# Performance work log

Measured on AMD Instinct MI355X. Metric: run time of the kernel, lower is better.

The kernel has to match this reference:

```python
import jax, jax.numpy as jnp
import numpy as np

ENT_FACTOR = 0.5  # entanglement_factor


def setup_inputs() -> dict:
    key = jax.random.key(0)
    k1, k2, k3, k4 = jax.random.split(key, 4)
    B, L, H, E = 2, 2048, 16, 128
    S = L
    return {
        "queries": jax.random.normal(k1, (B, L, H, E), dtype=jnp.float32),
        "keys": jax.random.normal(k2, (B, S, H, E), dtype=jnp.float32),
        "values": jax.random.normal(k3, (B, S, H, E), dtype=jnp.float32),
        "q_params": jax.random.uniform(k4, (4,), dtype=jnp.float32),
    }


def reference(queries, keys, values, q_params):
    B, L, H, E = queries.shape
    S = keys.shape[1]
    scale = 1.0 / jnp.sqrt(jnp.asarray(E, dtype=queries.dtype))
    # VQE circuit (RY layer, CNOT chain, <Z0>) reduces analytically to cos(theta0):
    # Z on the control qubit commutes with CNOT, so only RY(params[0]) matters.
    quantum_score = jnp.cos(q_params[0])
    # entanglement scores: values play the query role  -> [B,H,L,S]
    ent = jnp.einsum('blhd,bshd->bhls', values, keys)
    # NOTE: in QuantumAttentionOld classical QK scores are NOT added to `scores`.
    scores = quantum_score + ENT_FACTOR * ent
    causal = jnp.triu(jnp.ones((L, S), dtype=bool), k=1)  # True above diagonal
    scores = jnp.where(causal[None, None, :, :], -jnp.inf, scores)
    A = jax.nn.softmax(scale * scores, axis=-1)  # dropout is identity at eval
    V = jnp.einsum('bhls,bshd->blhd', A, values)
    return V
```

## Files before the change

### kernel.cpp

```cpp
#include <hip/hip_runtime.h>
#include <hip/hip_bf16.h>
#include <stdint.h>

#define LQ   2048
#define NH   16
#define DD   128
#define NB   2
#define QBLK 128
#define KBLK 64
#define NQT  (LQ/QBLK)
#define ROWSTR (NH*DD)

typedef float f32x4 __attribute__((ext_vector_type(4)));
typedef short s16x4 __attribute__((ext_vector_type(4)));
typedef short s16x8 __attribute__((ext_vector_type(8)));

__device__ __forceinline__ short f2bf(float f) {
  union { __hip_bfloat16 h; short s; } u;
  u.h = __float2bfloat16(f);
  return u.s;
}

__device__ __forceinline__ s16x4 cvt4(f32x4 x) {
  s16x4 r; r[0] = f2bf(x[0]); r[1] = f2bf(x[1]); r[2] = f2bf(x[2]); r[3] = f2bf(x[3]);
  return r;
}

__device__ __forceinline__ uint32_t lds_u32(const void* p) {
  return (uint32_t)(uint64_t)p;
}

__device__ __forceinline__ s16x4 tr16(uint32_t addr) {
  s16x4 d;
  asm volatile("ds_read_b64_tr_b16 %0, %1" : "=v"(d) : "v"(addr) : "memory");
  return d;
}

struct Stage { f32x4 k[4]; f32x4 v[4]; };

__device__ __forceinline__ Stage load_tile(const float* __restrict__ Kg,
                                           const float* __restrict__ Vg,
                                           int s0, int tid) {
  Stage st;
  const int rk = tid >> 5;
  const int c4 = tid & 31;
#pragma unroll
  for (int j = 0; j < 4; ++j)
    st.k[j] = *(const f32x4*)(Kg + (size_t)(s0 + rk + 16 * j) * ROWSTR + 4 * c4);
#pragma unroll
  for (int p = 0; p < 4; ++p) {
    const int g = tid + 512 * p;
    const int rv = (g & 3) | ((g >> 7) << 2);
    const int cv = (g >> 2) & 31;
    st.v[p] = *(const f32x4*)(Vg + (size_t)(s0 + rv) * ROWSTR + 4 * cv);
  }
  return st;
}

__device__ __forceinline__ void write_tile(short* Kb, short* Vb,
                                           const Stage& st, int tid) {
  const int rk = tid >> 5;
  const int c4 = tid & 31;
#pragma unroll
  for (int j = 0; j < 4; ++j)
    *(s16x4*)&Kb[(rk + 16 * j) * 132 + 4 * c4] = cvt4(st.k[j]);
#pragma unroll
  for (int p = 0; p < 4; ++p) {
    const int g = tid + 512 * p;
    const int rv = (g & 3) | ((g >> 7) << 2);
    const int cv = (g >> 2) & 31;
    const int sub = (rv >> 4) * 8 + (cv >> 2);
    *(s16x4*)&Vb[sub * 256 + (rv & 15) * 16 + 4 * (cv & 3)] = cvt4(st.v[p]);
  }
}

__global__ __launch_bounds__(512, 2) void qattn_fwd(
    const float* __restrict__ keys, const float* __restrict__ values,
    float* __restrict__ out)
{
  __shared__ short K_lds[2][KBLK * 132];
  __shared__ short V_lds[2][32 * 256];

  const int tid  = threadIdx.x;
  const int wid  = tid >> 6;
  const int lane = tid & 63;
  const int l15  = lane & 15;
  const int lhi  = lane >> 4;

  const int wg   = blockIdx.x;
  const int bh   = wg & 31;
  const int pair = wg >> 5;
  const int b    = bh >> 4;
  const int h    = bh & 15;

  const float* Kg = keys   + ((size_t)b * LQ * ROWSTR) + (size_t)h * DD;
  const float* Vg = values + ((size_t)b * LQ * ROWSTR) + (size_t)h * DD;
  float*       Og = out    + ((size_t)b * LQ * ROWSTR) + (size_t)h * DD;

  const float CS = 0.5f * 0.08838834764831845f * 1.4426950408889634f;

  for (int sp = 0; sp < 2; ++sp) {
    const int qt = sp ? (NQT - 1 - pair) : pair;
    const int q0 = qt * QBLK;
    const int nt = 2 * qt + 2;

    const int qg = q0 + wid * 16 + l15;
    const float* Qrow = Vg + (size_t)qg * ROWSTR;
    s16x8 qf[4];
#pragma unroll
    for (int c = 0; c < 4; ++c) {
      f32x4 lo = *(const f32x4*)(Qrow + 32 * c + 4 * lhi);
      f32x4 hi = *(const f32x4*)(Qrow + 32 * c + 16 + 4 * lhi);
      lo *= CS; hi *= CS;
      qf[c] = __builtin_shufflevector(cvt4(lo), cvt4(hi), 0, 1, 2, 3, 4, 5, 6, 7);
    }

    f32x4 o[8];
#pragma unroll
    for (int i = 0; i < 8; ++i) o[i] = f32x4{0.f, 0.f, 0.f, 0.f};
    float m  = -1e30f;
    float ll = 0.0f;
    const int q_wave_hi = q0 + wid * 16 + 15;

    {
      Stage st = load_tile(Kg, Vg, 0, tid);
      __syncthreads();
      write_tile(K_lds[0], V_lds[0], st, tid);
    }
    __syncthreads();

    for (int t = 0; t < nt; ++t) {
      const int cur = t & 1;
      const int s0  = t * KBLK;

      Stage st;
      const bool more = (t + 1) < nt;
      if (more) st = load_tile(Kg, Vg, (t + 1) * KBLK, tid);

      if (s0 <= q_wave_hi) {
        const short* Kb = K_lds[cur];
        short*       Vb = V_lds[cur];

        f32x4 sT[4];
#pragma unroll
        for (int sb = 0; sb < 4; ++sb) sT[sb] = f32x4{0.f, 0.f, 0.f, 0.f};
        __builtin_amdgcn_s_setprio(1);
#pragma unroll
        for (int c = 0; c < 4; ++c) {
#pragma unroll
          for (int sb = 0; sb < 4; ++sb) {
            s16x4 a = *(const s16x4*)&Kb[(sb * 16 + l15) * 132 + 32 * c + 4 * lhi];
            s16x4 bb = *(const s16x4*)&Kb[(sb * 16 + l15) * 132 + 32 * c + 16 + 4 * lhi];
            s16x8 kf = __builtin_shufflevector(a, bb, 0, 1, 2, 3, 4, 5, 6, 7);
            sT[sb] = __builtin_amdgcn_mfma_f32_16x16x32_bf16(kf, qf[c], sT[sb], 0, 0, 0);
          }
        }
        __builtin_amdgcn_s_setprio(0);

        float z[16];
#pragma unroll
        for (int sb = 0; sb < 4; ++sb)
#pragma unroll
          for (int r = 0; r < 4; ++r) z[sb * 4 + r] = sT[sb][r];
        if (s0 + KBLK - 1 > qg) {
#pragma unroll
          for (int sb = 0; sb < 4; ++sb)
#pragma unroll
            for (int r = 0; r < 4; ++r)
              if (s0 + sb * 16 + 4 * lhi + r > qg) z[sb * 4 + r] = -1e30f;
        }
        float tm = z[0];
#pragma unroll
        for (int i = 1; i < 16; ++i) tm = fmaxf(tm, z[i]);
        tm = fmaxf(tm, __shfl_xor(tm, 16));
        tm = fmaxf(tm, __shfl_xor(tm, 32));

        if (!__all(tm - m <= 8.0f)) {
          const float mn = fmaxf(m, tm);
          const float alpha = exp2f(m - mn);
          m = mn;
          float ar[4];
#pragma unroll
          for (int r = 0; r < 4; ++r) ar[r] = __shfl(alpha, 4 * lhi + r);
#pragma unroll
          for (int df = 0; df < 8; ++df)
#pragma unroll
            for (int r = 0; r < 4; ++r) o[df][r] *= ar[r];
          ll *= alpha;
        }
        float rs = 0.f;
        s16x8 pf0, pf1;
#pragma unroll
        for (int i = 0; i < 8; ++i) {
          float p = exp2f(z[i] - m);
          rs += p;
          pf0[i] = f2bf(p);
        }
#pragma unroll
        for (int i = 0; i < 8; ++i) {
          float p = exp2f(z[8 + i] - m);
          rs += p;
          pf1[i] = f2bf(p);
        }
        rs += __shfl_xor(rs, 16);
        rs += __shfl_xor(rs, 32);
        ll += rs;

        const uint32_t vbase = lds_u32(&Vb[0]) + 8u * (uint32_t)lane;
#pragma unroll
        for (int ks = 0; ks < 2; ++ks) {
          s16x4 vlo[8], vhi[8];
#pragma unroll
          for (int df = 0; df < 8; ++df) {
            vlo[df] = tr16(vbase + 512u * (uint32_t)(16 * ks + df));
            vhi[df] = tr16(vbase + 512u * (uint32_t)(16 * ks + 8 + df));
          }
          asm volatile("s_waitcnt lgkmcnt(0)" ::: "memory");
          __builtin_amdgcn_sched_barrier(0);
          const s16x8 pf = ks ? pf1 : pf0;
          __builtin_amdgcn_s_setprio(1);
#pragma unroll
          for (int df = 0; df < 8; ++df) {
            s16x8 vf = __builtin_shufflevector(vlo[df], vhi[df], 0, 1, 2, 3, 4, 5, 6, 7);
            o[df] = __builtin_amdgcn_mfma_f32_16x16x32_bf16(pf, vf, o[df], 0, 0, 0);
          }
          __builtin_amdgcn_s_setprio(0);
        }
      }

      if (more) write_tile(K_lds[cur ^ 1], V_lds[cur ^ 1], st, tid);
      __syncthreads();
    }

    const float linv = 1.0f / ll;
#pragma unroll
    for (int r = 0; r < 4; ++r) {
      const float lr = __shfl(linv, 4 * lhi + r);
      float* orow = Og + (size_t)(q0 + wid * 16 + 4 * lhi + r) * ROWSTR;
#pragma unroll
      for (int df = 0; df < 8; ++df)
        orow[df * 16 + l15] = o[df][r] * lr;
    }
  }
}

extern "C" void kernel_launch(void* const* d_in, const int* in_sizes, int n_in,
                              void* d_out, int out_size, void* d_ws, size_t ws_size,
                              hipStream_t stream) {
  const float* keys   = (const float*)d_in[1];
  const float* values = (const float*)d_in[2];
  float*       out    = (float*)d_out;
  dim3 grid(NB * NH * (NQT / 2));
  dim3 block(512);
  hipLaunchKernelGGL(qattn_fwd, grid, block, 0, stream, keys, values, out);
}
```

Baseline: 86.30 us.

## Split paired q-tiles into separate blocks, swizzle K LDS layout, raise occupancy

Each workgroup now processes a single query tile instead of a balanced pair, doubling the grid to 512 blocks. A custom ordering of block indices interleaves long and short causal tiles across heads to balance load. The K tile in LDS is permuted with a row stride of 136, so each lane reads its 8-element K fragment as one 16-byte load instead of two 8-byte loads. Launch bounds now request 4 blocks per CU, which limits registers per thread and risks spills. Load balance then depends on the hardware block scheduler rather than on the explicit pairing.

```diff
diff --git a/kernel.cpp b/kernel.cpp
--- a/kernel.cpp
+++ b/kernel.cpp
@@ -10,6 +10,7 @@
 #define KBLK 64
 #define NQT  (LQ/QBLK)
 #define ROWSTR (NH*DD)
+#define KROW 136
 
 typedef float f32x4 __attribute__((ext_vector_type(4)));
 typedef short s16x4 __attribute__((ext_vector_type(4)));
@@ -61,9 +62,10 @@
                                            const Stage& st, int tid) {
   const int rk = tid >> 5;
   const int c4 = tid & 31;
+  const int koff = (c4 >> 3) * 32 + (c4 & 3) * 8 + ((c4 >> 2) & 1) * 4;
 #pragma unroll
   for (int j = 0; j < 4; ++j)
-    *(s16x4*)&Kb[(rk + 16 * j) * 132 + 4 * c4] = cvt4(st.k[j]);
+    *(s16x4*)&Kb[(rk + 16 * j) * KROW + koff] = cvt4(st.k[j]);
 #pragma unroll
   for (int p = 0; p < 4; ++p) {
     const int g = tid + 512 * p;
@@ -74,11 +76,11 @@
   }
 }
 
-__global__ __launch_bounds__(512, 2) void qattn_fwd(
+__global__ __launch_bounds__(512, 4) void qattn_fwd(
     const float* __restrict__ keys, const float* __restrict__ values,
     float* __restrict__ out)
 {
-  __shared__ short K_lds[2][KBLK * 132];
+  __shared__ short K_lds[2][KBLK * KROW];
   __shared__ short V_lds[2][32 * 256];
 
   const int tid  = threadIdx.x;
@@ -87,11 +89,20 @@
   const int l15  = lane & 15;
   const int lhi  = lane >> 4;
 
-  const int wg   = blockIdx.x;
-  const int bh   = wg & 31;
-  const int pair = wg >> 5;
+  const int wg = blockIdx.x;
+  const int x  = wg & 7;
+  const int s  = wg >> 3;
+  {
+  }
+  const int u    = (s & 31) >> 1;
+  const int base = (s & 1) ? (15 - u) : u;
+  const int qt   = (s < 32) ? base : (15 - base);
+  const int rr   = ((s >= 32) ? 2 : 0) + (s & 1);
+  const int bh   = x + 8 * rr;
   const int b    = bh >> 4;
   const int h    = bh & 15;
+  const int q0   = qt * QBLK;
+  const int nt   = 2 * qt + 2;
 
   const float* Kg = keys   + ((size_t)b * LQ * ROWSTR) + (size_t)h * DD;
   const float* Vg = values + ((size_t)b * LQ * ROWSTR) + (size_t)h * DD;
@@ -99,148 +110,140 @@
 
   const float CS = 0.5f * 0.08838834764831845f * 1.4426950408889634f;
 
-  for (int sp = 0; sp < 2; ++sp) {
-    const int qt = sp ? (NQT - 1 - pair) : pair;
-    const int q0 = qt * QBLK;
-    const int nt = 2 * qt + 2;
-
-    const int qg = q0 + wid * 16 + l15;
-    const float* Qrow = Vg + (size_t)qg * ROWSTR;
-    s16x8 qf[4];
-#pragma unroll
-    for (int c = 0; c < 4; ++c) {
-      f32x4 lo = *(const f32x4*)(Qrow + 32 * c + 4 * lhi);
-      f32x4 hi = *(const f32x4*)(Qrow + 32 * c + 16 + 4 * lhi);
-      lo *= CS; hi *= CS;
-      qf[c] = __builtin_shufflevector(cvt4(lo), cvt4(hi), 0, 1, 2, 3, 4, 5, 6, 7);
+  const int qg = q0 + wid * 16 + l15;
+  const float* Qrow = Vg + (size_t)qg * ROWSTR;
+  s16x8 qf[4];
+#pragma unroll
+  for (int c = 0; c < 4; ++c) {
+    f32x4 lo = *(const f32x4*)(Qrow + 32 * c + 4 * lhi);
+    f32x4 hi = *(const f32x4*)(Qrow + 32 * c + 16 + 4 * lhi);
+    lo *= CS; hi *= CS;
+    qf[c] = __builtin_shufflevector(cvt4(lo), cvt4(hi), 0, 1, 2, 3, 4, 5, 6, 7);
+  }
+
+  f32x4 o[8];
+#pragma unroll
+  for (int i = 0; i < 8; ++i) o[i] = f32x4{0.f, 0.f, 0.f, 0.f};
+  float m  = -1e30f;
+  float ll = 0.0f;
+  const int q_wave_hi = q0 + wid * 16 + 15;
+
+  {
+    Stage st = load_tile(Kg, Vg, 0, tid);
+    write_tile(K_lds[0], V_lds[0], st, tid);
+  }
+  __syncthreads();
+
+  for (int t = 0; t < nt; ++t) {
+    const int cur = t & 1;
+    const int s0  = t * KBLK;
+
+    Stage st;
+    const bool more = (t + 1) < nt;
+    if (more) st = load_tile(Kg, Vg, (t + 1) * KBLK, tid);
+
+    if (s0 <= q_wave_hi) {
+      const short* Kb = K_lds[cur];
+      short*       Vb = V_lds[cur];
+
+      f32x4 sT[4];
+#pragma unroll
+      for (int sb = 0; sb < 4; ++sb) sT[sb] = f32x4{0.f, 0.f, 0.f, 0.f};
+      __builtin_amdgcn_s_setprio(1);
+#pragma unroll
+      for (int c = 0; c < 4; ++c) {
+#pragma unroll
+        for (int sb = 0; sb < 4; ++sb) {
+          s16x8 kf = *(const s16x8*)&Kb[(sb * 16 + l15) * KROW + c * 32 + lhi * 8];
+          sT[sb] = __builtin_amdgcn_mfma_f32_16x16x32_bf16(kf, qf[c], sT[sb], 0, 0, 0);
+        }
+      }
+      __builtin_amdgcn_s_setprio(0);
+
+      if (s0 + KBLK - 1 > qg) {
+#pragma unroll
+        for (int sb = 0; sb < 4; ++sb)
+#pragma unroll
+          for (int r = 0; r < 4; ++r)
+            if (s0 + sb * 16 + 4 * lhi + r > qg) sT[sb][r] = -1e30f;
+      }
+      float tm = sT[0][0];
+#pragma unroll
+      for (int sb = 0; sb < 4; ++sb)
+#pragma unroll
+        for (int r = 0; r < 4; ++r) tm = fmaxf(tm, sT[sb][r]);
+      tm = fmaxf(tm, __shfl_xor(tm, 16));
+      tm = fmaxf(tm, __shfl_xor(tm, 32));
+
+      if (!__all(tm - m <= 8.0f)) {
+        const float mn = fmaxf(m, tm);
+        const float alpha = exp2f(m - mn);
+        m = mn;
+        float ar[4];
+#pragma unroll
+        for (int r = 0; r < 4; ++r) ar[r] = __shfl(alpha, 4 * lhi + r);
+#pragma unroll
+        for (int df = 0; df < 8; ++df)
+#pragma unroll
+          for (int r = 0; r < 4; ++r) o[df][r] *= ar[r];
+        ll *= alpha;
+      }
+      float rs = 0.f;
+      s16x8 pf0, pf1;
+#pragma unroll
+      for (int sb = 0; sb < 2; ++sb)
+#pragma unroll
+        for (int r = 0; r < 4; ++r) {
+          float p = exp2f(sT[sb][r] - m);
+          rs += p;
+          pf0[sb * 4 + r] = f2bf(p);
+        }
+#pragma unroll
+      for (int sb = 0; sb < 2; ++sb)
+#pragma unroll
+        for (int r = 0; r < 4; ++r) {
+          float p = exp2f(sT[2 + sb][r] - m);
+          rs += p;
+          pf1[sb * 4 + r] = f2bf(p);
+        }
+      rs += __shfl_xor(rs, 16);
+      rs += __shfl_xor(rs, 32);
+      ll += rs;
+
+      const uint32_t vbase = lds_u32(&Vb[0]) + 8u * (uint32_t)lane;
+#pragma unroll
+      for (int ks = 0; ks < 2; ++ks) {
+        s16x4 vlo[8], vhi[8];
+#pragma unroll
+        for (int df = 0; df < 8; ++df) {
+          vlo[df] = tr16(vbase + 512u * (uint32_t)(16 * ks + df));
+          vhi[df] = tr16(vbase + 512u * (uint32_t)(16 * ks + 8 + df));
+        }
+        asm volatile("s_waitcnt lgkmcnt(0)" ::: "memory");
+        __builtin_amdgcn_sched_barrier(0);
+        const s16x8 pf = ks ? pf1 : pf0;
+        __builtin_amdgcn_s_setprio(1);
+#pragma unroll
+        for (int df = 0; df < 8; ++df) {
+          s16x8 vf = __builtin_shufflevector(vlo[df], vhi[df], 0, 1, 2, 3, 4, 5, 6, 7);
+          o[df] = __builtin_amdgcn_mfma_f32_16x16x32_bf16(pf, vf, o[df], 0, 0, 0);
+        }
+        __builtin_amdgcn_s_setprio(0);
+      }
     }
 
-    f32x4 o[8];
-#pragma unroll
-    for (int i = 0; i < 8; ++i) o[i] = f32x4{0.f, 0.f, 0.f, 0.f};
-    float m  = -1e30f;
-    float ll = 0.0f;
-    const int q_wave_hi = q0 + wid * 16 + 15;
-
-    {
-      Stage st = load_tile(Kg, Vg, 0, tid);
-      __syncthreads();
-      write_tile(K_lds[0], V_lds[0], st, tid);
-    }
+    if (more) write_tile(K_lds[cur ^ 1], V_lds[cur ^ 1], st, tid);
     __syncthreads();
-
-    for (int t = 0; t < nt; ++t) {
-      const int cur = t & 1;
-      const int s0  = t * KBLK;
-
-      Stage st;
-      const bool more = (t + 1) < nt;
-      if (more) st = load_tile(Kg, Vg, (t + 1) * KBLK, tid);
-
-      if (s0 <= q_wave_hi) {
-        const short* Kb = K_lds[cur];
-        short*       Vb = V_lds[cur];
-
-        f32x4 sT[4];
-#pragma unroll
-        for (int sb = 0; sb < 4; ++sb) sT[sb] = f32x4{0.f, 0.f, 0.f, 0.f};
-        __builtin_amdgcn_s_setprio(1);
-#pragma unroll
-        for (int c = 0; c < 4; ++c) {
-#pragma unroll
-          for (int sb = 0; sb < 4; ++sb) {
-            s16x4 a = *(const s16x4*)&Kb[(sb * 16 + l15) * 132 + 32 * c + 4 * lhi];
-            s16x4 bb = *(const s16x4*)&Kb[(sb * 16 + l15) * 132 + 32 * c + 16 + 4 * lhi];
-            s16x8 kf = __builtin_shufflevector(a, bb, 0, 1, 2, 3, 4, 5, 6, 7);
-            sT[sb] = __builtin_amdgcn_mfma_f32_16x16x32_bf16(kf, qf[c], sT[sb], 0, 0, 0);
-          }
-        }
-        __builtin_amdgcn_s_setprio(0);
-
-        float z[16];
-#pragma unroll
-        for (int sb = 0; sb < 4; ++sb)
-#pragma unroll
-          for (int r = 0; r < 4; ++r) z[sb * 4 + r] = sT[sb][r];
-        if (s0 + KBLK - 1 > qg) {
-#pragma unroll
-          for (int sb = 0; sb < 4; ++sb)
-#pragma unroll
-            for (int r = 0; r < 4; ++r)
-              if (s0 + sb * 16 + 4 * lhi + r > qg) z[sb * 4 + r] = -1e30f;
-        }
-        float tm = z[0];
-#pragma unroll
-        for (int i = 1; i < 16; ++i) tm = fmaxf(tm, z[i]);
-        tm = fmaxf(tm, __shfl_xor(tm, 16));
-        tm = fmaxf(tm, __shfl_xor(tm, 32));
-
-        if (!__all(tm - m <= 8.0f)) {
-          const float mn = fmaxf(m, tm);
-          const float alpha = exp2f(m - mn);
-          m = mn;
-          float ar[4];
-#pragma unroll
-          for (int r = 0; r < 4; ++r) ar[r] = __shfl(alpha, 4 * lhi + r);
-#pragma unroll
-          for (int df = 0; df < 8; ++df)
-#pragma unroll
-            for (int r = 0; r < 4; ++r) o[df][r] *= ar[r];
-          ll *= alpha;
-        }
-        float rs = 0.f;
-        s16x8 pf0, pf1;
-#pragma unroll
-        for (int i = 0; i < 8; ++i) {
-          float p = exp2f(z[i] - m);
-          rs += p;
-          pf0[i] = f2bf(p);
-        }
-#pragma unroll
-        for (int i = 0; i < 8; ++i) {
-          float p = exp2f(z[8 + i] - m);
-          rs += p;
-          pf1[i] = f2bf(p);
-        }
-        rs += __shfl_xor(rs, 16);
-        rs += __shfl_xor(rs, 32);
-        ll += rs;
-
-        const uint32_t vbase = lds_u32(&Vb[0]) + 8u * (uint32_t)lane;
-#pragma unroll
-        for (int ks = 0; ks < 2; ++ks) {
-          s16x4 vlo[8], vhi[8];
-#pragma unroll
-          for (int df = 0; df < 8; ++df) {
-            vlo[df] = tr16(vbase + 512u * (uint32_t)(16 * ks + df));
-            vhi[df] = tr16(vbase + 512u * (uint32_t)(16 * ks + 8 + df));
-          }
-          asm volatile("s_waitcnt lgkmcnt(0)" ::: "memory");
-          __builtin_amdgcn_sched_barrier(0);
-          const s16x8 pf = ks ? pf1 : pf0;
-          __builtin_amdgcn_s_setprio(1);
-#pragma unroll
-          for (int df = 0; df < 8; ++df) {
-            s16x8 vf = __builtin_shufflevector(vlo[df], vhi[df], 0, 1, 2, 3, 4, 5, 6, 7);
-            o[df] = __builtin_amdgcn_mfma_f32_16x16x32_bf16(pf, vf, o[df], 0, 0, 0);
-          }
-          __builtin_amdgcn_s_setprio(0);
-        }
-      }
-
-      if (more) write_tile(K_lds[cur ^ 1], V_lds[cur ^ 1], st, tid);
-      __syncthreads();
-    }
-
-    const float linv = 1.0f / ll;
-#pragma unroll
-    for (int r = 0; r < 4; ++r) {
-      const float lr = __shfl(linv, 4 * lhi + r);
-      float* orow = Og + (size_t)(q0 + wid * 16 + 4 * lhi + r) * ROWSTR;
-#pragma unroll
-      for (int df = 0; df < 8; ++df)
-        orow[df * 16 + l15] = o[df][r] * lr;
-    }
+  }
+
+  const float linv = 1.0f / ll;
+#pragma unroll
+  for (int r = 0; r < 4; ++r) {
+    const float lr = __shfl(linv, 4 * lhi + r);
+    float* orow = Og + (size_t)(q0 + wid * 16 + 4 * lhi + r) * ROWSTR;
+#pragma unroll
+    for (int df = 0; df < 8; ++df)
+      orow[df * 16 + l15] = o[df][r] * lr;
   }
 }
 
@@ -250,7 +253,7 @@
   const float* keys   = (const float*)d_in[1];
   const float* values = (const float*)d_in[2];
   float*       out    = (float*)d_out;
-  dim3 grid(NB * NH * (NQT / 2));
+  dim3 grid(2 * NB * NH * (NQT / 2));
   dim3 block(512);
   hipLaunchKernelGGL(qattn_fwd, grid, block, 0, stream, keys, values, out);
 }
```

Result: slower. 143.9 us (+66.8%).

## Split KV tile across two wave teams, each wave handling 32 queries

Applied to the files above, without the earlier changes.

The 8 waves are regrouped into two teams of four. Each wave now owns 32 query rows (two 16-row halves) and one 32-key half of each 64-key tile. Each K fragment and V fragment read from LDS therefore feeds two MFMAs, which halves the LDS read traffic per MFMA. The two teams' partial softmax states are merged at the end through LDS, which adds an extra sync and a combine step, plus more registers for the doubled accumulators.

```diff
diff --git a/kernel.cpp b/kernel.cpp
--- a/kernel.cpp
+++ b/kernel.cpp
@@ -10,6 +10,8 @@
 #define KBLK 64
 #define NQT  (LQ/QBLK)
 #define ROWSTR (NH*DD)
+#define KTILE (KBLK*132)
+#define VTILE (32*256)
 
 typedef float f32x4 __attribute__((ext_vector_type(4)));
 typedef short s16x4 __attribute__((ext_vector_type(4)));
@@ -78,14 +80,15 @@
     const float* __restrict__ keys, const float* __restrict__ values,
     float* __restrict__ out)
 {
-  __shared__ short K_lds[2][KBLK * 132];
-  __shared__ short V_lds[2][32 * 256];
+  __shared__ short SM[2 * KTILE + 2 * VTILE];
 
   const int tid  = threadIdx.x;
   const int wid  = tid >> 6;
   const int lane = tid & 63;
   const int l15  = lane & 15;
   const int lhi  = lane >> 4;
+  const int team = wid >> 2;
+  const int tw   = wid & 3;
 
   const int wg   = blockIdx.x;
   const int bh   = wg & 31;
@@ -98,148 +101,189 @@
   float*       Og = out    + ((size_t)b * LQ * ROWSTR) + (size_t)h * DD;
 
   const float CS = 0.5f * 0.08838834764831845f * 1.4426950408889634f;
+  const int soff = 32 * team;
 
   for (int sp = 0; sp < 2; ++sp) {
     const int qt = sp ? (NQT - 1 - pair) : pair;
     const int q0 = qt * QBLK;
     const int nt = 2 * qt + 2;
 
-    const int qg = q0 + wid * 16 + l15;
-    const float* Qrow = Vg + (size_t)qg * ROWSTR;
-    s16x8 qf[4];
-#pragma unroll
-    for (int c = 0; c < 4; ++c) {
-      f32x4 lo = *(const f32x4*)(Qrow + 32 * c + 4 * lhi);
-      f32x4 hi = *(const f32x4*)(Qrow + 32 * c + 16 + 4 * lhi);
-      lo *= CS; hi *= CS;
-      qf[c] = __builtin_shufflevector(cvt4(lo), cvt4(hi), 0, 1, 2, 3, 4, 5, 6, 7);
+    int qg[2];
+    s16x8 qf[2][4];
+#pragma unroll
+    for (int qh = 0; qh < 2; ++qh) {
+      qg[qh] = q0 + tw * 32 + qh * 16 + l15;
+      const float* Qrow = Vg + (size_t)qg[qh] * ROWSTR;
+#pragma unroll
+      for (int c = 0; c < 4; ++c) {
+        f32x4 lo = *(const f32x4*)(Qrow + 32 * c + 4 * lhi);
+        f32x4 hi = *(const f32x4*)(Qrow + 32 * c + 16 + 4 * lhi);
+        lo *= CS; hi *= CS;
+        qf[qh][c] = __builtin_shufflevector(cvt4(lo), cvt4(hi), 0, 1, 2, 3, 4, 5, 6, 7);
+      }
     }
 
-    f32x4 o[8];
-#pragma unroll
-    for (int i = 0; i < 8; ++i) o[i] = f32x4{0.f, 0.f, 0.f, 0.f};
-    float m  = -1e30f;
-    float ll = 0.0f;
-    const int q_wave_hi = q0 + wid * 16 + 15;
+    f32x4 o[2][8];
+#pragma unroll
+    for (int qh = 0; qh < 2; ++qh)
+#pragma unroll
+      for (int i = 0; i < 8; ++i) o[qh][i] = f32x4{0.f, 0.f, 0.f, 0.f};
+    float m[2]  = { -1e30f, -1e30f };
+    float ll[2] = { 0.f, 0.f };
+    const int q_wave_hi = q0 + tw * 32 + 31;
 
     {
       Stage st = load_tile(Kg, Vg, 0, tid);
-      __syncthreads();
-      write_tile(K_lds[0], V_lds[0], st, tid);
+      if (sp) __syncthreads();
+      write_tile(SM, SM + 2 * KTILE, st, tid);
     }
     __syncthreads();
 
     for (int t = 0; t < nt; ++t) {
       const int cur = t & 1;
-      const int s0  = t * KBLK;
+      const int s0t = t * KBLK + soff;
 
       Stage st;
       const bool more = (t + 1) < nt;
       if (more) st = load_tile(Kg, Vg, (t + 1) * KBLK, tid);
 
-      if (s0 <= q_wave_hi) {
-        const short* Kb = K_lds[cur];
-        short*       Vb = V_lds[cur];
-
-        f32x4 sT[4];
-#pragma unroll
-        for (int sb = 0; sb < 4; ++sb) sT[sb] = f32x4{0.f, 0.f, 0.f, 0.f};
+      if (s0t <= q_wave_hi) {
+        const short* Kb = SM + cur * KTILE;
+        const short* Vb = SM + 2 * KTILE + cur * VTILE;
+
+        f32x4 sT[2][2];
+#pragma unroll
+        for (int qh = 0; qh < 2; ++qh)
+#pragma unroll
+          for (int sb = 0; sb < 2; ++sb) sT[qh][sb] = f32x4{0.f, 0.f, 0.f, 0.f};
         __builtin_amdgcn_s_setprio(1);
 #pragma unroll
         for (int c = 0; c < 4; ++c) {
 #pragma unroll
-          for (int sb = 0; sb < 4; ++sb) {
-            s16x4 a = *(const s16x4*)&Kb[(sb * 16 + l15) * 132 + 32 * c + 4 * lhi];
-            s16x4 bb = *(const s16x4*)&Kb[(sb * 16 + l15) * 132 + 32 * c + 16 + 4 * lhi];
+          for (int sb = 0; sb < 2; ++sb) {
+            s16x4 a  = *(const s16x4*)&Kb[(soff + sb * 16 + l15) * 132 + 32 * c + 4 * lhi];
+            s16x4 bb = *(const s16x4*)&Kb[(soff + sb * 16 + l15) * 132 + 32 * c + 16 + 4 * lhi];
             s16x8 kf = __builtin_shufflevector(a, bb, 0, 1, 2, 3, 4, 5, 6, 7);
-            sT[sb] = __builtin_amdgcn_mfma_f32_16x16x32_bf16(kf, qf[c], sT[sb], 0, 0, 0);
+            sT[0][sb] = __builtin_amdgcn_mfma_f32_16x16x32_bf16(kf, qf[0][c], sT[0][sb], 0, 0, 0);
+            sT[1][sb] = __builtin_amdgcn_mfma_f32_16x16x32_bf16(kf, qf[1][c], sT[1][sb], 0, 0, 0);
           }
         }
         __builtin_amdgcn_s_setprio(0);
 
-        float z[16];
-#pragma unroll
-        for (int sb = 0; sb < 4; ++sb)
-#pragma unroll
-          for (int r = 0; r < 4; ++r) z[sb * 4 + r] = sT[sb][r];
-        if (s0 + KBLK - 1 > qg) {
-#pragma unroll
-          for (int sb = 0; sb < 4; ++sb)
-#pragma unroll
-            for (int r = 0; r < 4; ++r)
-              if (s0 + sb * 16 + 4 * lhi + r > qg) z[sb * 4 + r] = -1e30f;
-        }
-        float tm = z[0];
-#pragma unroll
-        for (int i = 1; i < 16; ++i) tm = fmaxf(tm, z[i]);
-        tm = fmaxf(tm, __shfl_xor(tm, 16));
-        tm = fmaxf(tm, __shfl_xor(tm, 32));
-
-        if (!__all(tm - m <= 8.0f)) {
-          const float mn = fmaxf(m, tm);
-          const float alpha = exp2f(m - mn);
-          m = mn;
-          float ar[4];
-#pragma unroll
-          for (int r = 0; r < 4; ++r) ar[r] = __shfl(alpha, 4 * lhi + r);
-#pragma unroll
-          for (int df = 0; df < 8; ++df)
-#pragma unroll
-            for (int r = 0; r < 4; ++r) o[df][r] *= ar[r];
-          ll *= alpha;
-        }
-        float rs = 0.f;
-        s16x8 pf0, pf1;
-#pragma unroll
-        for (int i = 0; i < 8; ++i) {
-          float p = exp2f(z[i] - m);
-          rs += p;
-          pf0[i] = f2bf(p);
-        }
-#pragma unroll
-        for (int i = 0; i < 8; ++i) {
-          float p = exp2f(z[8 + i] - m);
-          rs += p;
-          pf1[i] = f2bf(p);
-        }
-        rs += __shfl_xor(rs, 16);
-        rs += __shfl_xor(rs, 32);
-        ll += rs;
-
-        const uint32_t vbase = lds_u32(&Vb[0]) + 8u * (uint32_t)lane;
-#pragma unroll
-        for (int ks = 0; ks < 2; ++ks) {
-          s16x4 vlo[8], vhi[8];
-#pragma unroll
-          for (int df = 0; df < 8; ++df) {
-            vlo[df] = tr16(vbase + 512u * (uint32_t)(16 * ks + df));
-            vhi[df] = tr16(vbase + 512u * (uint32_t)(16 * ks + 8 + df));
-          }
-          asm volatile("s_waitcnt lgkmcnt(0)" ::: "memory");
-          __builtin_amdgcn_sched_barrier(0);
-          const s16x8 pf = ks ? pf1 : pf0;
-          __builtin_amdgcn_s_setprio(1);
-#pragma unroll
-          for (int df = 0; df < 8; ++df) {
-            s16x8 vf = __builtin_shufflevector(vlo[df], vhi[df], 0, 1, 2, 3, 4, 5, 6, 7);
-            o[df] = __builtin_amdgcn_mfma_f32_16x16x32_bf16(pf, vf, o[df], 0, 0, 0);
-          }
-          __builtin_amdgcn_s_setprio(0);
-        }
+        const uint32_t vbase = lds_u32(Vb) + 8u * (uint32_t)lane
+                             + 512u * (uint32_t)(16 * team);
+        s16x4 vlo[8], vhi[8];
+#pragma unroll
+        for (int df = 0; df < 8; ++df) {
+          vlo[df] = tr16(vbase + 512u * (uint32_t)df);
+          vhi[df] = tr16(vbase + 512u * (uint32_t)(8 + df));
+        }
+
+        s16x8 pf[2];
+#pragma unroll
+        for (int qh = 0; qh < 2; ++qh) {
+          if (s0t + 31 > qg[qh]) {
+#pragma unroll
+            for (int sb = 0; sb < 2; ++sb)
+#pragma unroll
+              for (int r = 0; r < 4; ++r)
+                if (s0t + sb * 16 + 4 * lhi + r > qg[qh]) sT[qh][sb][r] = -1e30f;
+          }
+          float tm = sT[qh][0][0];
+#pragma unroll
+          for (int sb = 0; sb < 2; ++sb)
+#pragma unroll
+            for (int r = 0; r < 4; ++r) tm = fmaxf(tm, sT[qh][sb][r]);
+          tm = fmaxf(tm, __shfl_xor(tm, 16));
+          tm = fmaxf(tm, __shfl_xor(tm, 32));
+
+          if (!__all(tm - m[qh] <= 8.0f)) {
+            const float mn = fmaxf(m[qh], tm);
+            const float alpha = exp2f(m[qh] - mn);
+            m[qh] = mn;
+            float ar[4];
+#pragma unroll
+            for (int r = 0; r < 4; ++r) ar[r] = __shfl(alpha, 4 * lhi + r);
+#pragma unroll
+            for (int df = 0; df < 8; ++df)
+#pragma unroll
+              for (int r = 0; r < 4; ++r) o[qh][df][r] *= ar[r];
+            ll[qh] *= alpha;
+          }
+          float rs = 0.f;
+#pragma unroll
+          for (int sb = 0; sb < 2; ++sb)
+#pragma unroll
+            for (int r = 0; r < 4; ++r) {
+              float p = exp2f(sT[qh][sb][r] - m[qh]);
+              rs += p;
+              pf[qh][sb * 4 + r] = f2bf(p);
+            }
+          rs += __shfl_xor(rs, 16);
+          rs += __shfl_xor(rs, 32);
+          ll[qh] += rs;
+        }
+
+        asm volatile("s_waitcnt lgkmcnt(0)" ::: "memory");
+        __builtin_amdgcn_sched_barrier(0);
+        __builtin_amdgcn_s_setprio(1);
+#pragma unroll
+        for (int df = 0; df < 8; ++df) {
+          s16x8 vf = __builtin_shufflevector(vlo[df], vhi[df], 0, 1, 2, 3, 4, 5, 6, 7);
+          o[0][df] = __builtin_amdgcn_mfma_f32_16x16x32_bf16(pf[0], vf, o[0][df], 0, 0, 0);
+          o[1][df] = __builtin_amdgcn_mfma_f32_16x16x32_bf16(pf[1], vf, o[1][df], 0, 0, 0);
+        }
+        __builtin_amdgcn_s_setprio(0);
       }
 
-      if (more) write_tile(K_lds[cur ^ 1], V_lds[cur ^ 1], st, tid);
+      if (more) write_tile(SM + (cur ^ 1) * KTILE,
+                           SM + 2 * KTILE + (cur ^ 1) * VTILE, st, tid);
       __syncthreads();
     }
 
-    const float linv = 1.0f / ll;
-#pragma unroll
-    for (int r = 0; r < 4; ++r) {
-      const float lr = __shfl(linv, 4 * lhi + r);
-      float* orow = Og + (size_t)(q0 + wid * 16 + 4 * lhi + r) * ROWSTR;
-#pragma unroll
-      for (int df = 0; df < 8; ++df)
-        orow[df * 16 + l15] = o[df][r] * lr;
+    {
+      float* LM_O  = (float*)SM;
+      float* LM_ml = (float*)SM + 128 * 128;
+      if (team == 1) {
+#pragma unroll
+        for (int qh = 0; qh < 2; ++qh) {
+#pragma unroll
+          for (int r = 0; r < 4; ++r) {
+            const int qloc = tw * 32 + qh * 16 + 4 * lhi + r;
+#pragma unroll
+            for (int df = 0; df < 8; ++df)
+              LM_O[qloc * 128 + df * 16 + l15] = o[qh][df][r];
+          }
+          if (lhi == 0) {
+            LM_ml[tw * 32 + qh * 16 + l15]       = m[qh];
+            LM_ml[128 + tw * 32 + qh * 16 + l15] = ll[qh];
+          }
+        }
+      }
+      __syncthreads();
+      if (team == 0) {
+#pragma unroll
+        for (int qh = 0; qh < 2; ++qh) {
+#pragma unroll
+          for (int r = 0; r < 4; ++r) {
+            const int qloc = tw * 32 + qh * 16 + 4 * lhi + r;
+            const float mA = __shfl(m[qh], 4 * lhi + r);
+            const float lA = __shfl(ll[qh], 4 * lhi + r);
+            const float mB = LM_ml[qloc];
+            const float lB = LM_ml[128 + qloc];
+            const float ms = fmaxf(mA, mB);
+            const float aA = exp2f(mA - ms);
+            const float aB = exp2f(mB - ms);
+            const float inv = 1.0f / (lA * aA + lB * aB);
+            const float cA = aA * inv, cB = aB * inv;
+            float* orow = Og + (size_t)(q0 + qloc) * ROWSTR;
+#pragma unroll
+            for (int df = 0; df < 8; ++df)
+              orow[df * 16 + l15] = o[qh][df][r] * cA
+                                  + LM_O[qloc * 128 + df * 16 + l15] * cB;
+          }
+        }
+      }
     }
   }
 }
```

Result: slower. 90.38 us (+4.7%).

## Double KV tile to 128 rows, split K/V prefetch, skip masked diagonal subtiles

Applied to the files above, without the earlier changes.

Raises the key/value tile from 64 to 128 rows so each block runs half as many loop iterations and barriers. K and V global prefetches are split, with V loaded after the QK MFMAs and K written to LDS before softmax, so fewer registers are live at once. On the diagonal tile, each wave skips QK and PV subtiles that lie entirely above the causal boundary. The cost is more shared memory and registers, and launch bounds drop to one block per SIMD pair, which reduces occupancy.

```diff
diff --git a/kernel.cpp b/kernel.cpp
--- a/kernel.cpp
+++ b/kernel.cpp
@@ -7,9 +7,11 @@
 #define DD   128
 #define NB   2
 #define QBLK 128
-#define KBLK 64
+#define KBLK 128
 #define NQT  (LQ/QBLK)
 #define ROWSTR (NH*DD)
+#define KTILE (KBLK*132)
+#define VTILE (64*256)
 
 typedef float f32x4 __attribute__((ext_vector_type(4)));
 typedef short s16x4 __attribute__((ext_vector_type(4)));
@@ -36,19 +38,31 @@
   return d;
 }
 
-struct Stage { f32x4 k[4]; f32x4 v[4]; };
-
-__device__ __forceinline__ Stage load_tile(const float* __restrict__ Kg,
-                                           const float* __restrict__ Vg,
-                                           int s0, int tid) {
-  Stage st;
+struct KStage { f32x4 k[8]; };
+struct VStage { f32x4 v[8]; };
+
+__device__ __forceinline__ KStage loadK(const float* __restrict__ Kg, int s0, int tid) {
+  KStage st;
   const int rk = tid >> 5;
   const int c4 = tid & 31;
 #pragma unroll
-  for (int j = 0; j < 4; ++j)
+  for (int j = 0; j < 8; ++j)
     st.k[j] = *(const f32x4*)(Kg + (size_t)(s0 + rk + 16 * j) * ROWSTR + 4 * c4);
-#pragma unroll
-  for (int p = 0; p < 4; ++p) {
+  return st;
+}
+
+__device__ __forceinline__ void writeK(short* Kb, const KStage& st, int tid) {
+  const int rk = tid >> 5;
+  const int c4 = tid & 31;
+#pragma unroll
+  for (int j = 0; j < 8; ++j)
+    *(s16x4*)&Kb[(rk + 16 * j) * 132 + 4 * c4] = cvt4(st.k[j]);
+}
+
+__device__ __forceinline__ VStage loadV(const float* __restrict__ Vg, int s0, int tid) {
+  VStage st;
+#pragma unroll
+  for (int p = 0; p < 8; ++p) {
     const int g = tid + 512 * p;
     const int rv = (g & 3) | ((g >> 7) << 2);
     const int cv = (g >> 2) & 31;
@@ -57,15 +71,9 @@
   return st;
 }
 
-__device__ __forceinline__ void write_tile(short* Kb, short* Vb,
-                                           const Stage& st, int tid) {
-  const int rk = tid >> 5;
-  const int c4 = tid & 31;
-#pragma unroll
-  for (int j = 0; j < 4; ++j)
-    *(s16x4*)&Kb[(rk + 16 * j) * 132 + 4 * c4] = cvt4(st.k[j]);
-#pragma unroll
-  for (int p = 0; p < 4; ++p) {
+__device__ __forceinline__ void writeV(short* Vb, const VStage& st, int tid) {
+#pragma unroll
+  for (int p = 0; p < 8; ++p) {
     const int g = tid + 512 * p;
     const int rv = (g & 3) | ((g >> 7) << 2);
     const int cv = (g >> 2) & 31;
@@ -74,12 +82,11 @@
   }
 }
 
-__global__ __launch_bounds__(512, 2) void qattn_fwd(
+__global__ __launch_bounds__(512, 1) void qattn_fwd(
     const float* __restrict__ keys, const float* __restrict__ values,
     float* __restrict__ out)
 {
-  __shared__ short K_lds[2][KBLK * 132];
-  __shared__ short V_lds[2][32 * 256];
+  __shared__ short SM[2 * KTILE + 2 * VTILE];
 
   const int tid  = threadIdx.x;
   const int wid  = tid >> 6;
@@ -102,7 +109,7 @@
   for (int sp = 0; sp < 2; ++sp) {
     const int qt = sp ? (NQT - 1 - pair) : pair;
     const int q0 = qt * QBLK;
-    const int nt = 2 * qt + 2;
+    const int nt = qt + 1;
 
     const int qg = q0 + wid * 16 + l15;
     const float* Qrow = Vg + (size_t)qg * ROWSTR;
@@ -120,95 +127,99 @@
     for (int i = 0; i < 8; ++i) o[i] = f32x4{0.f, 0.f, 0.f, 0.f};
     float m  = -1e30f;
     float ll = 0.0f;
-    const int q_wave_hi = q0 + wid * 16 + 15;
 
     {
-      Stage st = load_tile(Kg, Vg, 0, tid);
-      __syncthreads();
-      write_tile(K_lds[0], V_lds[0], st, tid);
+      KStage kst = loadK(Kg, 0, tid);
+      VStage vst = loadV(Vg, 0, tid);
+      writeK(SM, kst, tid);
+      writeV(SM + 2 * KTILE, vst, tid);
     }
     __syncthreads();
 
     for (int t = 0; t < nt; ++t) {
       const int cur = t & 1;
       const int s0  = t * KBLK;
-
-      Stage st;
       const bool more = (t + 1) < nt;
-      if (more) st = load_tile(Kg, Vg, (t + 1) * KBLK, tid);
-
-      if (s0 <= q_wave_hi) {
-        const short* Kb = K_lds[cur];
-        short*       Vb = V_lds[cur];
-
-        f32x4 sT[4];
-#pragma unroll
-        for (int sb = 0; sb < 4; ++sb) sT[sb] = f32x4{0.f, 0.f, 0.f, 0.f};
-        __builtin_amdgcn_s_setprio(1);
-#pragma unroll
-        for (int c = 0; c < 4; ++c) {
-#pragma unroll
-          for (int sb = 0; sb < 4; ++sb) {
-            s16x4 a = *(const s16x4*)&Kb[(sb * 16 + l15) * 132 + 32 * c + 4 * lhi];
+      const bool diag = (t == nt - 1);
+
+      const short* Kb = SM + cur * KTILE;
+      const short* Vb = SM + 2 * KTILE + cur * VTILE;
+      short* Kn = SM + (cur ^ 1) * KTILE;
+      short* Vn = SM + 2 * KTILE + (cur ^ 1) * VTILE;
+
+      KStage kst;
+      if (more) kst = loadK(Kg, (t + 1) * KBLK, tid);
+
+      f32x4 sT[8];
+#pragma unroll
+      for (int sb = 0; sb < 8; ++sb) sT[sb] = f32x4{0.f, 0.f, 0.f, 0.f};
+      __builtin_amdgcn_s_setprio(1);
+#pragma unroll
+      for (int sb = 0; sb < 8; ++sb) {
+        if (!diag || sb <= wid) {
+#pragma unroll
+          for (int c = 0; c < 4; ++c) {
+            s16x4 a  = *(const s16x4*)&Kb[(sb * 16 + l15) * 132 + 32 * c + 4 * lhi];
             s16x4 bb = *(const s16x4*)&Kb[(sb * 16 + l15) * 132 + 32 * c + 16 + 4 * lhi];
             s16x8 kf = __builtin_shufflevector(a, bb, 0, 1, 2, 3, 4, 5, 6, 7);
             sT[sb] = __builtin_amdgcn_mfma_f32_16x16x32_bf16(kf, qf[c], sT[sb], 0, 0, 0);
           }
         }
-        __builtin_amdgcn_s_setprio(0);
-
-        float z[16];
-#pragma unroll
-        for (int sb = 0; sb < 4; ++sb)
-#pragma unroll
-          for (int r = 0; r < 4; ++r) z[sb * 4 + r] = sT[sb][r];
-        if (s0 + KBLK - 1 > qg) {
-#pragma unroll
-          for (int sb = 0; sb < 4; ++sb)
-#pragma unroll
-            for (int r = 0; r < 4; ++r)
-              if (s0 + sb * 16 + 4 * lhi + r > qg) z[sb * 4 + r] = -1e30f;
-        }
-        float tm = z[0];
-#pragma unroll
-        for (int i = 1; i < 16; ++i) tm = fmaxf(tm, z[i]);
-        tm = fmaxf(tm, __shfl_xor(tm, 16));
-        tm = fmaxf(tm, __shfl_xor(tm, 32));
-
-        if (!__all(tm - m <= 8.0f)) {
-          const float mn = fmaxf(m, tm);
-          const float alpha = exp2f(m - mn);
-          m = mn;
-          float ar[4];
-#pragma unroll
-          for (int r = 0; r < 4; ++r) ar[r] = __shfl(alpha, 4 * lhi + r);
-#pragma unroll
-          for (int df = 0; df < 8; ++df)
-#pragma unroll
-            for (int r = 0; r < 4; ++r) o[df][r] *= ar[r];
-          ll *= alpha;
-        }
-        float rs = 0.f;
-        s16x8 pf0, pf1;
-#pragma unroll
-        for (int i = 0; i < 8; ++i) {
-          float p = exp2f(z[i] - m);
-          rs += p;
-          pf0[i] = f2bf(p);
-        }
-#pragma unroll
-        for (int i = 0; i < 8; ++i) {
-          float p = exp2f(z[8 + i] - m);
-          rs += p;
-          pf1[i] = f2bf(p);
-        }
-        rs += __shfl_xor(rs, 16);
-        rs += __shfl_xor(rs, 32);
-        ll += rs;
-
-        const uint32_t vbase = lds_u32(&Vb[0]) + 8u * (uint32_t)lane;
-#pragma unroll
-        for (int ks = 0; ks < 2; ++ks) {
+      }
+      __builtin_amdgcn_s_setprio(0);
+
+      VStage vst;
+      if (more) vst = loadV(Vg, (t + 1) * KBLK, tid);
+      if (more) writeK(Kn, kst, tid);
+
+      if (diag) {
+#pragma unroll
+        for (int sb = 0; sb < 8; ++sb)
+#pragma unroll
+          for (int r = 0; r < 4; ++r)
+            if (s0 + sb * 16 + 4 * lhi + r > qg) sT[sb][r] = -1e30f;
+      }
+      float mx[16];
+#pragma unroll
+      for (int i = 0; i < 16; ++i) mx[i] = fmaxf(sT[i >> 1][(i & 1) * 2], sT[i >> 1][(i & 1) * 2 + 1]);
+#pragma unroll
+      for (int i = 0; i < 8; ++i) mx[i] = fmaxf(mx[2 * i], mx[2 * i + 1]);
+#pragma unroll
+      for (int i = 0; i < 4; ++i) mx[i] = fmaxf(mx[2 * i], mx[2 * i + 1]);
+      float tm = fmaxf(fmaxf(mx[0], mx[1]), fmaxf(mx[2], mx[3]));
+      tm = fmaxf(tm, __shfl_xor(tm, 16));
+      tm = fmaxf(tm, __shfl_xor(tm, 32));
+
+      if (!__all(tm - m <= 8.0f)) {
+        const float mn = fmaxf(m, tm);
+        const float alpha = exp2f(m - mn);
+        m = mn;
+        float ar[4];
+#pragma unroll
+        for (int r = 0; r < 4; ++r) ar[r] = __shfl(alpha, 4 * lhi + r);
+#pragma unroll
+        for (int df = 0; df < 8; ++df)
+#pragma unroll
+          for (int r = 0; r < 4; ++r) o[df][r] *= ar[r];
+        ll *= alpha;
+      }
+      float rs = 0.f;
+      s16x8 pf[4];
+#pragma unroll
+      for (int ks = 0; ks < 4; ++ks)
+#pragma unroll
+        for (int sb = 0; sb < 2; ++sb)
+#pragma unroll
+          for (int r = 0; r < 4; ++r) {
+            float p = exp2f(sT[2 * ks + sb][r] - m);
+            rs += p;
+            pf[ks][sb * 4 + r] = f2bf(p);
+          }
+
+      const uint32_t vbase = lds_u32(Vb) + 8u * (uint32_t)lane;
+#pragma unroll
+      for (int ks = 0; ks < 4; ++ks) {
+        if (!diag || ks <= (wid >> 1)) {
           s16x4 vlo[8], vhi[8];
 #pragma unroll
           for (int df = 0; df < 8; ++df) {
@@ -217,18 +228,22 @@
           }
           asm volatile("s_waitcnt lgkmcnt(0)" ::: "memory");
           __builtin_amdgcn_sched_barrier(0);
-          const s16x8 pf = ks ? pf1 : pf0;
           __builtin_amdgcn_s_setprio(1);
 #pragma unroll
           for (int df = 0; df < 8; ++df) {
             s16x8 vf = __builtin_shufflevector(vlo[df], vhi[df], 0, 1, 2, 3, 4, 5, 6, 7);
-            o[df] = __builtin_amdgcn_mfma_f32_16x16x32_bf16(pf, vf, o[df], 0, 0, 0);
+            o[df] = __builtin_amdgcn_mfma_f32_16x16x32_bf16(pf[ks], vf, o[df], 0, 0, 0);
           }
           __builtin_amdgcn_s_setprio(0);
         }
       }
 
-      if (more) write_tile(K_lds[cur ^ 1], V_lds[cur ^ 1], st, tid);
+      if (more) writeV(Vn, vst, tid);
+
+      rs += __shfl_xor(rs, 16);
+      rs += __shfl_xor(rs, 32);
+      ll += rs;
+
       __syncthreads();
     }
 
```

Measured after the change: 185.8 us. 2.15x slower.
